# Optimization experiments

Measured on AMD Instinct MI355X. Metric: run time of the kernel, lower is better.

The kernel has to match this reference:

```python
import jax, jax.numpy as jnp
import numpy as np

N = 100_000      # nodes
E = 1_600_000    # directed edges (before self-loops)
G = 128          # graphs in batch
IN = 32          # in_channels
HID = 32         # hidden_channels (per head)
HEADS = 4
SLOPE = 0.2      # GATConv leaky_relu negative_slope


def setup_inputs() -> dict:
    key = jax.random.key(0)
    ks = jax.random.split(key, 12)
    x = jax.random.normal(ks[0], (N, IN), jnp.float32)
    edge_index = jax.random.randint(ks[1], (2, E), 0, N)
    batch = jnp.sort(jax.random.randint(ks[2], (N,), 0, G))
    g = lambda k, sh: jax.random.normal(k, sh, jnp.float32) * (1.0 / np.sqrt(sh[0]))
    return {
        "x": x, "edge_index": edge_index, "batch": batch,
        # conv1: in -> heads*hid, concat
        "W1": g(ks[3], (IN, HEADS * HID)),
        "a_src1": jax.random.normal(ks[4], (HEADS, HID), jnp.float32) * 0.1,
        "a_dst1": jax.random.normal(ks[5], (HEADS, HID), jnp.float32) * 0.1,
        "b1": jnp.zeros((HEADS * HID,), jnp.float32),
        # conv2: heads*hid -> hid, heads=1, mean (concat=False)
        "W2": g(ks[6], (HEADS * HID, 1 * HID)),
        "a_src2": jax.random.normal(ks[7], (1, HID), jnp.float32) * 0.1,
        "a_dst2": jax.random.normal(ks[8], (1, HID), jnp.float32) * 0.1,
        "b2": jnp.zeros((HID,), jnp.float32),
        # classifier
        "Wc": g(ks[9], (HID, 1)),
        "bc": jnp.zeros((1,), jnp.float32),
    }


def _segment_softmax(e, seg, n):
    # e: [E', H]; softmax over edges sharing the same destination node
    m = jax.ops.segment_max(e, seg, num_segments=n)
    ex = jnp.exp(e - m[seg])
    den = jax.ops.segment_sum(ex, seg, num_segments=n)
    return ex / den[seg]


def _gat_layer(x, src, dst, W, a_src, a_dst, b, heads, ch, concat):
    n = x.shape[0]
    h = (x @ W).reshape(n, heads, ch)              # [N, H, C]
    e_src = jnp.sum(h * a_src, axis=-1)            # [N, H]
    e_dst = jnp.sum(h * a_dst, axis=-1)            # [N, H]
    e = jax.nn.leaky_relu(e_src[src] + e_dst[dst], SLOPE)   # [E', H]
    alpha = _segment_softmax(e, dst, n)            # [E', H]
    msg = h[src] * alpha[:, :, None]               # [E', H, C]
    out = jax.ops.segment_sum(msg, dst, num_segments=n)     # [N, H, C]
    out = out.reshape(n, heads * ch) if concat else out.mean(axis=1)
    return out + b


def reference(x, edge_index, batch, W1, a_src1, a_dst1, b1, W2, a_src2, a_dst2, b2, Wc, bc):
    n = x.shape[0]
    loops = jnp.arange(n, dtype=edge_index.dtype)  # GATConv add_self_loops=True
    src = jnp.concatenate([edge_index[0], loops])
    dst = jnp.concatenate([edge_index[1], loops])
    h = jax.nn.elu(_gat_layer(x, src, dst, W1, a_src1, a_dst1, b1, HEADS, HID, True))
    # dropout: eval mode -> identity
    h = jax.nn.elu(_gat_layer(h, src, dst, W2, a_src2, a_dst2, b2, 1, HID, False))
    # global_mean_pool over batch ids
    sums = jax.ops.segment_sum(h, batch, num_segments=G)
    cnt = jax.ops.segment_sum(jnp.ones((n, 1), h.dtype), batch, num_segments=G)
    pooled = sums / jnp.maximum(cnt, 1.0)
    return pooled @ Wc + bc                        # [G, 1]
```

## Files before the change

### kernel.cpp

```cpp
#include <hip/hip_runtime.h>
#include <math.h>

#define NT 100000
#define ET 1600000
#define GT 128
#define NBK 391
#define BSH 8
#define NBLK_A 256
#define CHUNK_A 6250

typedef float f4 __attribute__((ext_vector_type(4)));

__device__ __forceinline__ float lrelu(float v) { return v > 0.0f ? v : 0.2f * v; }
__device__ __forceinline__ float elu1(float v) { return v > 0.0f ? v : __expf(v) - 1.0f; }

__global__ __launch_bounds__(256) void k_histA(const int* __restrict__ dst, int* __restrict__ histA) {
  __shared__ int histL[NBK];
  int t = threadIdx.x, blk = blockIdx.x;
  for (int i = t; i < NBK; i += 256) histL[i] = 0;
  __syncthreads();
  int e0 = blk * CHUNK_A, e1 = min(ET, e0 + CHUNK_A);
  for (int e = e0 + t; e < e1; e += 256) atomicAdd(&histL[dst[e] >> BSH], 1);
  __syncthreads();
  for (int i = t; i < NBK; i += 256) histA[i * NBLK_A + blk] = histL[i];
}

__global__ __launch_bounds__(256) void k_scanB(int* __restrict__ histA, int* __restrict__ btot) {
  __shared__ int sh[256];
  int b = blockIdx.x, t = threadIdx.x;
  int v = histA[b * NBLK_A + t];
  sh[t] = v;
  __syncthreads();
  for (int off = 1; off < 256; off <<= 1) {
    int xv = (t >= off) ? sh[t - off] : 0;
    __syncthreads();
    sh[t] += xv;
    __syncthreads();
  }
  histA[b * NBLK_A + t] = sh[t] - v;
  if (t == 255) btot[b] = sh[255];
}

__global__ __launch_bounds__(512) void k_scanC(const int* __restrict__ btot, int* __restrict__ bbase) {
  __shared__ int sh[512];
  int t = threadIdx.x;
  int v = (t < NBK) ? btot[t] : 0;
  sh[t] = v;
  __syncthreads();
  for (int off = 1; off < 512; off <<= 1) {
    int xv = (t >= off) ? sh[t - off] : 0;
    __syncthreads();
    sh[t] += xv;
    __syncthreads();
  }
  if (t < NBK) bbase[t] = sh[t] - v;
  if (t == 0) bbase[NBK] = ET;
}

__global__ __launch_bounds__(256) void k_buck(const int* __restrict__ src, const int* __restrict__ dst,
                                              const int* __restrict__ histA, const int* __restrict__ bbase,
                                              unsigned int* __restrict__ ebuf) {
  __shared__ int cur[NBK];
  int t = threadIdx.x, blk = blockIdx.x;
  for (int i = t; i < NBK; i += 256) cur[i] = histA[i * NBLK_A + blk] + bbase[i];
  __syncthreads();
  int e0 = blk * CHUNK_A, e1 = min(ET, e0 + CHUNK_A);
  for (int e = e0 + t; e < e1; e += 256) {
    unsigned int s = (unsigned int)src[e];
    int d = dst[e];
    int pos = atomicAdd(&cur[d >> BSH], 1);
    ebuf[pos] = ((unsigned int)(d & 255) << 17) | s;
  }
}

__global__ __launch_bounds__(256) void k_fine(const unsigned int* __restrict__ ebuf, const int* __restrict__ bbase,
                                              int* __restrict__ rp, int* __restrict__ adj) {
  __shared__ int cnt[256];
  __shared__ int sh[256];
  __shared__ int cur[256];
  int b = blockIdx.x, t = threadIdx.x;
  int eb0 = bbase[b], eb1 = bbase[b + 1];
  cnt[t] = 0;
  __syncthreads();
  for (int e = eb0 + t; e < eb1; e += 256) atomicAdd(&cnt[ebuf[e] >> 17], 1);
  __syncthreads();
  int v = cnt[t];
  sh[t] = v;
  __syncthreads();
  for (int off = 1; off < 256; off <<= 1) {
    int xv = (t >= off) ? sh[t - off] : 0;
    __syncthreads();
    sh[t] += xv;
    __syncthreads();
  }
  int start = eb0 + sh[t] - v;
  cur[t] = start;
  int node = (b << BSH) + t;
  if (node < NT) rp[node] = start;
  if (node == NT - 1) rp[NT] = ET;
  __syncthreads();
  for (int e = eb0 + t; e < eb1; e += 256) {
    unsigned int p = ebuf[e];
    int pos = atomicAdd(&cur[p >> 17], 1);
    adj[pos] = (int)(p & 0x1FFFFu);
  }
}

__global__ void k_prep(const float* __restrict__ W1, const float* __restrict__ as1,
                       const float* __restrict__ ad1, float* __restrict__ AB) {
  int t = threadIdx.x;
  int k = t >> 3, j = t & 7;
  const float* a = (j < 4) ? as1 : ad1;
  int h = j & 3;
  float s = 0.0f;
  for (int c = 0; c < 32; ++c) s += W1[k * 128 + h * 32 + c] * a[h * 32 + c];
  AB[t] = s;
}

__global__ __launch_bounds__(256) void k_att1(const float* __restrict__ x, const float* __restrict__ AB,
                                              float* __restrict__ es, float* __restrict__ ed) {
  __shared__ float xsh[32 * 33];
  __shared__ float absh[256];
  int t = threadIdx.x;
  int n0 = blockIdx.x * 32;
  absh[t] = AB[t];
  for (int i = t; i < 1024; i += 256) {
    int ln = i >> 5, k = i & 31;
    int node = n0 + ln;
    xsh[ln * 33 + k] = (node < NT) ? x[node * 32 + k] : 0.0f;
  }
  __syncthreads();
  int ln = t >> 3, j = t & 7;
  int node = n0 + ln;
  if (node < NT) {
    float s = 0.0f;
#pragma unroll
    for (int k = 0; k < 32; ++k) s += xsh[ln * 33 + k] * absh[k * 8 + j];
    if (j < 4) es[node * 4 + j] = s;
    else ed[node * 4 + (j - 4)] = s;
  }
}

__global__ __launch_bounds__(256) void k_agg1g(
    const int* __restrict__ rp, const int* __restrict__ adj,
    const float* __restrict__ es, const float* __restrict__ ed,
    const float* __restrict__ x, float* __restrict__ y) {
  __shared__ int sbuf[8][34];
  __shared__ f4 wbufv[8][34];
  int t = threadIdx.x;
  int wv = t >> 6, l = t & 63;
  int g = l >> 5, j = l & 31;
  int ns = wv * 2 + g;
  int n = blockIdx.x * 8 + ns;
  bool valid = (n < NT);
  int nc = valid ? n : NT - 1;
  const f4* es4 = (const f4*)es;
  int rs = rp[nc], re = rp[nc + 1];
  int deg = re - rs;
  f4 edn = ((const f4*)ed)[nc];
  f4 esn = es4[nc];
  float sv[4];
#pragma unroll
  for (int h = 0; h < 4; ++h) sv[h] = __expf(lrelu(esn[h] + edn[h]));
  int eg2 = j >> 3, q = j & 7;
  f4 a0 = {0,0,0,0}, a1 = {0,0,0,0}, a2 = {0,0,0,0}, a3 = {0,0,0,0};

  if (deg <= 32) {
    float ex[4] = {0.0f, 0.0f, 0.0f, 0.0f};
    if (j < deg) {
      int s = adj[rs + j];
      sbuf[ns][j] = s;
      f4 ev = es4[s];
#pragma unroll
      for (int h = 0; h < 4; ++h) ex[h] = __expf(lrelu(ev[h] + edn[h]));
    }
    float d[4] = {ex[0], ex[1], ex[2], ex[3]};
#pragma unroll
    for (int off = 1; off <= 16; off <<= 1)
#pragma unroll
      for (int h = 0; h < 4; ++h) d[h] += __shfl_xor(d[h], off);
    float inv[4];
#pragma unroll
    for (int h = 0; h < 4; ++h) inv[h] = 1.0f / (d[h] + sv[h]);
    if (j < deg) {
      f4 w4;
#pragma unroll
      for (int h = 0; h < 4; ++h) w4[h] = ex[h] * inv[h];
      wbufv[ns][j] = w4;
    }
    if (j == 0) {
      sbuf[ns][deg] = nc;
      f4 w4;
#pragma unroll
      for (int h = 0; h < 4; ++h) w4[h] = sv[h] * inv[h];
      wbufv[ns][deg] = w4;
    }
    __builtin_amdgcn_wave_barrier();
    for (int e = eg2; e <= deg; e += 4) {
      f4 xv = *(const f4*)&x[sbuf[ns][e] * 32 + 4 * q];
      f4 w4 = wbufv[ns][e];
      a0 += w4.x * xv; a1 += w4.y * xv; a2 += w4.z * xv; a3 += w4.w * xv;
    }
  } else {
    float d[4] = {0.0f, 0.0f, 0.0f, 0.0f};
    for (int jj = rs + j; jj < re; jj += 32) {
      f4 ev = es4[adj[jj]];
#pragma unroll
      for (int h = 0; h < 4; ++h) d[h] += __expf(lrelu(ev[h] + edn[h]));
    }
#pragma unroll
    for (int off = 1; off <= 16; off <<= 1)
#pragma unroll
      for (int h = 0; h < 4; ++h) d[h] += __shfl_xor(d[h], off);
    float inv[4];
#pragma unroll
    for (int h = 0; h < 4; ++h) inv[h] = 1.0f / (d[h] + sv[h]);
    for (int base = rs; base < re; base += 32) {
      int cnt = min(32, re - base);
      if (j < cnt) {
        int s = adj[base + j];
        sbuf[ns][j] = s;
        f4 ev = es4[s];
        f4 w4;
#pragma unroll
        for (int h = 0; h < 4; ++h) w4[h] = __expf(lrelu(ev[h] + edn[h])) * inv[h];
        wbufv[ns][j] = w4;
      }
      __builtin_amdgcn_wave_barrier();
      for (int e = eg2; e < cnt; e += 4) {
        f4 xv = *(const f4*)&x[sbuf[ns][e] * 32 + 4 * q];
        f4 w4 = wbufv[ns][e];
        a0 += w4.x * xv; a1 += w4.y * xv; a2 += w4.z * xv; a3 += w4.w * xv;
      }
      __builtin_amdgcn_wave_barrier();
    }
    if (eg2 == 0) {
      f4 xv = *(const f4*)&x[nc * 32 + 4 * q];
      a0 += sv[0] * inv[0] * xv; a1 += sv[1] * inv[1] * xv;
      a2 += sv[2] * inv[2] * xv; a3 += sv[3] * inv[3] * xv;
    }
  }

#pragma unroll
  for (int off = 8; off <= 16; off <<= 1) {
#pragma unroll
    for (int cc = 0; cc < 4; ++cc) {
      a0[cc] += __shfl_xor(a0[cc], off);
      a1[cc] += __shfl_xor(a1[cc], off);
      a2[cc] += __shfl_xor(a2[cc], off);
      a3[cc] += __shfl_xor(a3[cc], off);
    }
  }
  if (eg2 == 0 && valid) {
    *(f4*)&y[n * 128 + 0 * 32 + 4 * q] = a0;
    *(f4*)&y[n * 128 + 1 * 32 + 4 * q] = a1;
    *(f4*)&y[n * 128 + 2 * 32 + 4 * q] = a2;
    *(f4*)&y[n * 128 + 3 * 32 + 4 * q] = a3;
  }
}

__global__ __launch_bounds__(256) void k_mv(
    const float* __restrict__ y,
    const float* __restrict__ W1, const float* __restrict__ b1,
    const float* __restrict__ W2,
    const float* __restrict__ as2, const float* __restrict__ ad2,
    float* __restrict__ h2, float* __restrict__ es2, float* __restrict__ ed2) {
  __shared__ float W1sh[4096];
  __shared__ float W2t[32 * 132];
  __shared__ float b1sh[128];
  __shared__ float ysh[32][132];
  __shared__ float osh[32][132];
  int t = threadIdx.x;
  int n0 = blockIdx.x * 32;
  for (int i = t; i < 4096; i += 256) {
    float w = W1[i];
    W1sh[i] = w;
    float w2 = W2[i];
    int k = i >> 5, c = i & 31;
    W2t[c * 132 + k] = w2;
  }
  if (t < 128) b1sh[t] = b1[t];
  for (int i = t; i < 4096; i += 256) {
    int nd = i >> 7, c = i & 127;
    int node = n0 + nd;
    ysh[nd][(c >> 5) * 33 + (c & 31)] = (node < NT) ? y[node * 128 + c] : 0.0f;
  }
  __syncthreads();

  int j2 = t & 31, grp = t >> 5;
  int h = j2 >> 3;
  float as2v = as2[j2], ad2v = ad2[j2];
#pragma unroll
  for (int i = 0; i < 4; ++i) {
    int nd = grp * 4 + i;
    int node = n0 + nd;
    f4 o = {0, 0, 0, 0};
#pragma unroll
    for (int k = 0; k < 32; ++k) {
      o += ysh[nd][h * 33 + k] * *(const f4*)&W1sh[k * 128 + 4 * j2];
    }
    o += *(const f4*)&b1sh[4 * j2];
#pragma unroll
    for (int cc = 0; cc < 4; ++cc) o[cc] = elu1(o[cc]);
    *(f4*)&osh[nd][4 * j2] = o;
    __builtin_amdgcn_wave_barrier();
    float p = 0.0f;
#pragma unroll
    for (int k4 = 0; k4 < 128; k4 += 4) {
      f4 ov = *(const f4*)&osh[nd][k4];
      f4 wv = *(const f4*)&W2t[j2 * 132 + k4];
      p += ov.x * wv.x + ov.y * wv.y + ov.z * wv.z + ov.w * wv.w;
    }
    float ps = p * as2v, pd = p * ad2v;
#pragma unroll
    for (int off = 1; off <= 16; off <<= 1) {
      ps += __shfl_xor(ps, off);
      pd += __shfl_xor(pd, off);
    }
    if (node < NT) {
      h2[node * 32 + j2] = p;
      if (j2 == 0) { es2[node] = ps; ed2[node] = pd; }
    }
    __builtin_amdgcn_wave_barrier();
  }
}

__global__ __launch_bounds__(256) void k_agg2(const int* __restrict__ rp, const int* __restrict__ adj,
                                              const float* __restrict__ es, const float* __restrict__ ed,
                                              const float* __restrict__ h, const float* __restrict__ b2,
                                              const float* __restrict__ Wc, float* __restrict__ z) {
  __shared__ int sbuf[8][34];
  __shared__ float wsh[8][34];
  int t = threadIdx.x;
  int wv = t >> 6, l = t & 63;
  int g = l >> 5, j = l & 31;
  int ns = wv * 2 + g;
  int n = blockIdx.x * 8 + ns;
  if (n >= NT) return;
  int rs = rp[n], re = rp[n + 1];
  int deg = re - rs;
  float edn = ed[n];
  float sv = __expf(lrelu(es[n] + edn));
  int eg2 = j >> 3, q = j & 7;
  f4 acc = {0,0,0,0};

  if (deg <= 32) {
    float ex = 0.0f;
    if (j < deg) {
      int s = adj[rs + j];
      sbuf[ns][j] = s;
      ex = __expf(lrelu(es[s] + edn));
    }
    float d = ex;
#pragma unroll
    for (int off = 1; off <= 16; off <<= 1) d += __shfl_xor(d, off);
    float inv = 1.0f / (d + sv);
    if (j < deg) wsh[ns][j] = ex * inv;
    if (j == 0) { sbuf[ns][deg] = n; wsh[ns][deg] = sv * inv; }
    __builtin_amdgcn_wave_barrier();
    for (int e = eg2; e <= deg; e += 4) {
      acc += wsh[ns][e] * *(const f4*)&h[sbuf[ns][e] * 32 + 4 * q];
    }
  } else {
    float d = 0.0f;
    for (int jj = rs + j; jj < re; jj += 32) d += __expf(lrelu(es[adj[jj]] + edn));
#pragma unroll
    for (int off = 1; off <= 16; off <<= 1) d += __shfl_xor(d, off);
    float inv = 1.0f / (d + sv);
    for (int base = rs; base < re; base += 32) {
      int cnt = min(32, re - base);
      if (j < cnt) {
        int s = adj[base + j];
        sbuf[ns][j] = s;
        wsh[ns][j] = __expf(lrelu(es[s] + edn)) * inv;
      }
      __builtin_amdgcn_wave_barrier();
      for (int e = eg2; e < cnt; e += 4) {
        acc += wsh[ns][e] * *(const f4*)&h[sbuf[ns][e] * 32 + 4 * q];
      }
      __builtin_amdgcn_wave_barrier();
    }
    if (eg2 == 0) acc += sv * inv * *(const f4*)&h[n * 32 + 4 * q];
  }

#pragma unroll
  for (int off = 8; off <= 16; off <<= 1)
#pragma unroll
    for (int cc = 0; cc < 4; ++cc) acc[cc] += __shfl_xor(acc[cc], off);
  if (eg2 == 0) {
    f4 o = acc + *(const f4*)&b2[4 * q];
#pragma unroll
    for (int cc = 0; cc < 4; ++cc) o[cc] = elu1(o[cc]);
    f4 wc = *(const f4*)&Wc[4 * q];
    float zz = o.x * wc.x + o.y * wc.y + o.z * wc.z + o.w * wc.w;
#pragma unroll
    for (int off = 1; off <= 4; off <<= 1) zz += __shfl_xor(zz, off);
    if (q == 0) z[n] = zz;
  }
}

__global__ __launch_bounds__(256) void k_poolz(const float* __restrict__ z, const int* __restrict__ batch,
                                               const float* __restrict__ bc, float* __restrict__ out) {
  int g = blockIdx.x;
  int lo = 0, hi = NT;
  while (lo < hi) { int mid = (lo + hi) >> 1; if (batch[mid] < g) lo = mid + 1; else hi = mid; }
  int start = lo;
  hi = NT;
  while (lo < hi) { int mid = (lo + hi) >> 1; if (batch[mid] < g + 1) lo = mid + 1; else hi = mid; }
  int end = lo;

  int t = threadIdx.x;
  float s = 0.0f;
  for (int n = start + t; n < end; n += 256) s += z[n];
#pragma unroll
  for (int off = 1; off <= 32; off <<= 1) s += __shfl_xor(s, off);
  __shared__ float sh[4];
  if ((t & 63) == 0) sh[t >> 6] = s;
  __syncthreads();
  if (t == 0) {
    float tot = sh[0] + sh[1] + sh[2] + sh[3];
    float cnt = (float)(end - start);
    out[g] = tot / fmaxf(cnt, 1.0f) + bc[0];
  }
}

extern "C" void kernel_launch(void* const* d_in, const int* in_sizes, int n_in,
                              void* d_out, int out_size, void* d_ws, size_t ws_size,
                              hipStream_t stream) {
  const float* x = (const float*)d_in[0];
  const int* ei = (const int*)d_in[1];
  const int* src = ei;
  const int* dst = ei + ET;
  const int* batch = (const int*)d_in[2];
  const float* W1 = (const float*)d_in[3];
  const float* asrc1 = (const float*)d_in[4];
  const float* adst1 = (const float*)d_in[5];
  const float* b1 = (const float*)d_in[6];
  const float* W2 = (const float*)d_in[7];
  const float* asrc2 = (const float*)d_in[8];
  const float* adst2 = (const float*)d_in[9];
  const float* b2 = (const float*)d_in[10];
  const float* Wc = (const float*)d_in[11];
  const float* bc = (const float*)d_in[12];
  float* out = (float*)d_out;
  char* ws = (char*)d_ws;

  int* row_ptr = (int*)(ws + 0);
  int* histA = (int*)(ws + 400128);
  int* btot = (int*)(ws + 800512);
  int* bbase = (int*)(ws + 802112);
  float* AB = (float*)(ws + 803712);
  unsigned int* ebuf = (unsigned int*)(ws + 804736);
  int* adj = (int*)(ws + 7204736);
  float* es1 = (float*)(ws + 13604736);
  float* ed1 = (float*)(ws + 15204736);
  float* es2 = (float*)(ws + 16804736);
  float* ed2 = (float*)(ws + 17204736);
  float* h2 = (float*)(ws + 17604736);
  float* z = (float*)(ws + 30404736);
  float* y = (float*)(ws + 30804736);

  k_histA<<<NBLK_A, 256, 0, stream>>>(dst, histA);
  k_scanB<<<NBK, 256, 0, stream>>>(histA, btot);
  k_scanC<<<1, 512, 0, stream>>>(btot, bbase);
  k_buck<<<NBLK_A, 256, 0, stream>>>(src, dst, histA, bbase, ebuf);
  k_fine<<<NBK, 256, 0, stream>>>(ebuf, bbase, row_ptr, adj);

  k_prep<<<1, 256, 0, stream>>>(W1, asrc1, adst1, AB);
  k_att1<<<(NT + 31) / 32, 256, 0, stream>>>(x, AB, es1, ed1);

  k_agg1g<<<(NT + 7) / 8, 256, 0, stream>>>(row_ptr, adj, es1, ed1, x, y);

  k_mv<<<(NT + 31) / 32, 256, 0, stream>>>(y, W1, b1, W2, asrc2, adst2, h2, es2, ed2);

  k_agg2<<<(NT + 7) / 8, 256, 0, stream>>>(row_ptr, adj, es2, ed2, h2, b2, Wc, z);

  k_poolz<<<GT, 256, 0, stream>>>(z, batch, bc, out);
}
```

Baseline: 242.8 us.

## Restructure node-wise matmul kernel and unroll gather loops in aggregation kernels

Replaces k_mv with k_mv2, which no longer stages W1/W2 into shared memory. Each thread now owns one node and a 16-column slice, reading the weights straight from global/cache into register tiles. Per-node reductions go through a transposed shared buffer, and es2/ed2 are computed by 32 threads instead of shuffle reductions. The gather loops in k_agg1g and k_agg2 for low-degree nodes are unrolled four-way to keep more loads in flight. Out-of-range nodes now exit early instead of being clamped, and k_mv2 drops its bounds checks because NT divides evenly by 32.

Result: slower. 261.2 us (+7.6%).

```diff
diff --git a/kernel.cpp b/kernel.cpp
--- a/kernel.cpp
+++ b/kernel.cpp
@@ -152,13 +152,12 @@
   int g = l >> 5, j = l & 31;
   int ns = wv * 2 + g;
   int n = blockIdx.x * 8 + ns;
-  bool valid = (n < NT);
-  int nc = valid ? n : NT - 1;
+  if (n >= NT) return;
   const f4* es4 = (const f4*)es;
-  int rs = rp[nc], re = rp[nc + 1];
+  int rs = rp[n], re = rp[n + 1];
   int deg = re - rs;
-  f4 edn = ((const f4*)ed)[nc];
-  f4 esn = es4[nc];
+  f4 edn = ((const f4*)ed)[n];
+  f4 esn = es4[n];
   float sv[4];
 #pragma unroll
   for (int h = 0; h < 4; ++h) sv[h] = __expf(lrelu(esn[h] + edn[h]));
@@ -189,17 +188,23 @@
       wbufv[ns][j] = w4;
     }
     if (j == 0) {
-      sbuf[ns][deg] = nc;
+      sbuf[ns][deg] = n;
       f4 w4;
 #pragma unroll
       for (int h = 0; h < 4; ++h) w4[h] = sv[h] * inv[h];
       wbufv[ns][deg] = w4;
     }
     __builtin_amdgcn_wave_barrier();
-    for (int e = eg2; e <= deg; e += 4) {
-      f4 xv = *(const f4*)&x[sbuf[ns][e] * 32 + 4 * q];
-      f4 w4 = wbufv[ns][e];
-      a0 += w4.x * xv; a1 += w4.y * xv; a2 += w4.z * xv; a3 += w4.w * xv;
+    for (int e0 = eg2; e0 <= deg; e0 += 16) {
+#pragma unroll
+      for (int i = 0; i < 4; ++i) {
+        int e = e0 + i * 4;
+        if (e <= deg) {
+          f4 xv = *(const f4*)&x[sbuf[ns][e] * 32 + 4 * q];
+          f4 w4 = wbufv[ns][e];
+          a0 += w4.x * xv; a1 += w4.y * xv; a2 += w4.z * xv; a3 += w4.w * xv;
+        }
+      }
     }
   } else {
     float d[4] = {0.0f, 0.0f, 0.0f, 0.0f};
@@ -235,7 +240,7 @@
       __builtin_amdgcn_wave_barrier();
     }
     if (eg2 == 0) {
-      f4 xv = *(const f4*)&x[nc * 32 + 4 * q];
+      f4 xv = *(const f4*)&x[n * 32 + 4 * q];
       a0 += sv[0] * inv[0] * xv; a1 += sv[1] * inv[1] * xv;
       a2 += sv[2] * inv[2] * xv; a3 += sv[3] * inv[3] * xv;
     }
@@ -251,7 +256,7 @@
       a3[cc] += __shfl_xor(a3[cc], off);
     }
   }
-  if (eg2 == 0 && valid) {
+  if (eg2 == 0) {
     *(f4*)&y[n * 128 + 0 * 32 + 4 * q] = a0;
     *(f4*)&y[n * 128 + 1 * 32 + 4 * q] = a1;
     *(f4*)&y[n * 128 + 2 * 32 + 4 * q] = a2;
@@ -259,69 +264,71 @@
   }
 }
 
-__global__ __launch_bounds__(256) void k_mv(
+__global__ __launch_bounds__(256) void k_mv2(
     const float* __restrict__ y,
     const float* __restrict__ W1, const float* __restrict__ b1,
     const float* __restrict__ W2,
     const float* __restrict__ as2, const float* __restrict__ ad2,
     float* __restrict__ h2, float* __restrict__ es2, float* __restrict__ ed2) {
-  __shared__ float W1sh[4096];
-  __shared__ float W2t[32 * 132];
-  __shared__ float b1sh[128];
-  __shared__ float ysh[32][132];
-  __shared__ float osh[32][132];
+  __shared__ float ysh[128][33];
+  __shared__ float osh[128][33];
+  __shared__ float psh[32][37];
   int t = threadIdx.x;
   int n0 = blockIdx.x * 32;
-  for (int i = t; i < 4096; i += 256) {
-    float w = W1[i];
-    W1sh[i] = w;
-    float w2 = W2[i];
-    int k = i >> 5, c = i & 31;
-    W2t[c * 132 + k] = w2;
-  }
-  if (t < 128) b1sh[t] = b1[t];
-  for (int i = t; i < 4096; i += 256) {
-    int nd = i >> 7, c = i & 127;
-    int node = n0 + nd;
-    ysh[nd][(c >> 5) * 33 + (c & 31)] = (node < NT) ? y[node * 128 + c] : 0.0f;
-  }
-  __syncthreads();
-
-  int j2 = t & 31, grp = t >> 5;
-  int h = j2 >> 3;
-  float as2v = as2[j2], ad2v = ad2[j2];
+  for (int it = t; it < 4096; it += 256) {
+    int nd = it >> 7, c = it & 127;
+    ysh[c][nd] = y[(n0 + nd) * 128 + c];
+  }
+  __syncthreads();
+
+  int nd = t & 31, cq = t >> 5;
+  int h = cq >> 1;
+  f4 o4[4];
+#pragma unroll
+  for (int i = 0; i < 4; ++i) o4[i] = *(const f4*)&b1[cq * 16 + 4 * i];
+#pragma unroll 4
+  for (int k = 0; k < 32; ++k) {
+    float yv = ysh[h * 32 + k][nd];
+#pragma unroll
+    for (int i = 0; i < 4; ++i) {
+      f4 wv = *(const f4*)&W1[k * 128 + cq * 16 + 4 * i];
+      o4[i] += yv * wv;
+    }
+  }
 #pragma unroll
   for (int i = 0; i < 4; ++i) {
-    int nd = grp * 4 + i;
-    int node = n0 + nd;
-    f4 o = {0, 0, 0, 0};
-#pragma unroll
-    for (int k = 0; k < 32; ++k) {
-      o += ysh[nd][h * 33 + k] * *(const f4*)&W1sh[k * 128 + 4 * j2];
-    }
-    o += *(const f4*)&b1sh[4 * j2];
-#pragma unroll
-    for (int cc = 0; cc < 4; ++cc) o[cc] = elu1(o[cc]);
-    *(f4*)&osh[nd][4 * j2] = o;
-    __builtin_amdgcn_wave_barrier();
-    float p = 0.0f;
-#pragma unroll
-    for (int k4 = 0; k4 < 128; k4 += 4) {
-      f4 ov = *(const f4*)&osh[nd][k4];
-      f4 wv = *(const f4*)&W2t[j2 * 132 + k4];
-      p += ov.x * wv.x + ov.y * wv.y + ov.z * wv.z + ov.w * wv.w;
-    }
-    float ps = p * as2v, pd = p * ad2v;
-#pragma unroll
-    for (int off = 1; off <= 16; off <<= 1) {
-      ps += __shfl_xor(ps, off);
-      pd += __shfl_xor(pd, off);
-    }
-    if (node < NT) {
-      h2[node * 32 + j2] = p;
-      if (j2 == 0) { es2[node] = ps; ed2[node] = pd; }
-    }
-    __builtin_amdgcn_wave_barrier();
+#pragma unroll
+    for (int cc = 0; cc < 4; ++cc) {
+      int c = cq * 16 + 4 * i + cc;
+      osh[c][nd] = elu1(o4[i][cc]);
+    }
+  }
+  __syncthreads();
+
+  f4 p = {0, 0, 0, 0};
+#pragma unroll 8
+  for (int k = 0; k < 128; ++k) {
+    float ov = osh[k][nd];
+    p += ov * *(const f4*)&W2[k * 32 + cq * 4];
+  }
+  *(f4*)&psh[nd][cq * 4] = p;
+  __syncthreads();
+
+  {
+    int nd2 = t >> 3, i8 = t & 7;
+    f4 pv = *(const f4*)&psh[nd2][i8 * 4];
+    *(f4*)&h2[(n0 + nd2) * 32 + i8 * 4] = pv;
+  }
+  if (t < 32) {
+    float ps = 0.0f, pd = 0.0f;
+#pragma unroll 8
+    for (int c = 0; c < 32; ++c) {
+      float pv = psh[t][c];
+      ps += pv * as2[c];
+      pd += pv * ad2[c];
+    }
+    es2[n0 + t] = ps;
+    ed2[n0 + t] = pd;
   }
 }
 
@@ -358,8 +365,14 @@
     if (j < deg) wsh[ns][j] = ex * inv;
     if (j == 0) { sbuf[ns][deg] = n; wsh[ns][deg] = sv * inv; }
     __builtin_amdgcn_wave_barrier();
-    for (int e = eg2; e <= deg; e += 4) {
-      acc += wsh[ns][e] * *(const f4*)&h[sbuf[ns][e] * 32 + 4 * q];
+    for (int e0 = eg2; e0 <= deg; e0 += 16) {
+#pragma unroll
+      for (int i = 0; i < 4; ++i) {
+        int e = e0 + i * 4;
+        if (e <= deg) {
+          acc += wsh[ns][e] * *(const f4*)&h[sbuf[ns][e] * 32 + 4 * q];
+        }
+      }
     }
   } else {
     float d = 0.0f;
@@ -471,7 +484,7 @@
 
   k_agg1g<<<(NT + 7) / 8, 256, 0, stream>>>(row_ptr, adj, es1, ed1, x, y);
 
-  k_mv<<<(NT + 31) / 32, 256, 0, stream>>>(y, W1, b1, W2, asrc2, adst2, h2, es2, ed2);
+  k_mv2<<<NT / 32, 256, 0, stream>>>(y, W1, b1, W2, asrc2, adst2, h2, es2, ed2);
 
   k_agg2<<<(NT + 7) / 8, 256, 0, stream>>>(row_ptr, adj, es2, ed2, h2, b2, Wc, z);
 
```
